# Performance work log

Measured on AMD Instinct MI355X. Metric: run time of the kernel, lower is better.

The kernel has to match this reference:

```python
import jax, jax.numpy as jnp
import numpy as np

D_MODEL = 1024
H = 16
D_K = D_MODEL // H


def setup_inputs() -> dict:
    key = jax.random.key(0)
    ks = jax.random.split(key, 12)
    b, nq, nk = 2, 2048, 2048
    inp = {
        "queries": jax.random.normal(ks[0], (b, nq, D_MODEL), jnp.float32),
        "keys": jax.random.normal(ks[1], (b, nk, D_MODEL), jnp.float32),
        "values": jax.random.normal(ks[2], (b, nk, D_MODEL), jnp.float32),
        "query_mask": jax.random.uniform(ks[3], (b, nq), jnp.float32),
        "key_mask": jax.random.uniform(ks[4], (b, nk), jnp.float32),
        "attention_mask": jax.random.randint(ks[5], (b, 1, nq, nk), 0, 2).astype(bool),
        "attention_weights": jax.random.uniform(ks[6], (b, 1, nq, nk), jnp.float32),
        # Linear params init: normal(std=0.001) weights, zero bias (per init_weights)
        "Wq": 0.001 * jax.random.normal(ks[7], (D_MODEL, D_MODEL), jnp.float32),
        "Wk": 0.001 * jax.random.normal(ks[8], (D_MODEL, D_MODEL), jnp.float32),
        "Wv": 0.001 * jax.random.normal(ks[9], (D_MODEL, D_MODEL), jnp.float32),
        "Wo": 0.001 * jax.random.normal(ks[10], (D_MODEL, D_MODEL), jnp.float32),
        "bq": jnp.zeros((D_MODEL,), jnp.float32),
        "bk": jnp.zeros((D_MODEL,), jnp.float32),
        "bv": jnp.zeros((D_MODEL,), jnp.float32),
        "bo": jnp.zeros((D_MODEL,), jnp.float32),
    }
    return inp


def reference(queries, keys, values, query_mask, key_mask, attention_mask,
              attention_weights, Wq, Wk, Wv, Wo, bq, bk, bv, bo):
    b, nq, _ = queries.shape
    nk = keys.shape[1]
    # projections (torch Linear: x @ W.T + b)
    q = (queries @ Wq.T + bq).reshape(b, nq, H, D_K).transpose(0, 2, 1, 3)  # bhqd
    k = (keys @ Wk.T + bk).reshape(b, nk, H, D_K).transpose(0, 2, 1, 3)    # bhkd
    v = (values @ Wv.T + bv).reshape(b, nk, H, D_K).transpose(0, 2, 1, 3)  # bhkd
    # multiplicative per-token masks
    q = q * query_mask[:, None, :, None]
    k = k * key_mask[:, None, :, None]
    v = v * key_mask[:, None, :, None]
    att = jnp.einsum('bhqd,bhkd->bhqk', q, k) / np.sqrt(D_K).astype(np.float32)
    att = att * attention_weights
    att = jnp.where(attention_mask, -jnp.inf, att)
    att_softmax = jax.nn.softmax(att, axis=-1)
    # dropout is identity in eval/reference mode
    out = jnp.einsum('bhqk,bhkd->bhqd', att_softmax, v)
    out = out.transpose(0, 2, 1, 3).reshape(b, nq, H * D_K)
    out_final = out @ Wo.T + bo
    return (out_final, att_softmax)
```

## Files before the change

kernel.cpp:

```cpp
#include <hip/hip_runtime.h>

#define B2 2
#define NQ 2048
#define NK 2048
#define DM 1024
#define NH 16
#define DK 64
#define KC 64

typedef unsigned short u16;
typedef __attribute__((ext_vector_type(8))) short bf16x8;
typedef __attribute__((ext_vector_type(4))) float f32x4;

__device__ __forceinline__ u16 f2bf(float f) {
  unsigned u = __float_as_uint(f);
  u += 0x7FFFu + ((u >> 16) & 1u);
  return (u16)(u >> 16);
}
__device__ __forceinline__ float bf2f(u16 u) {
  return __uint_as_float(((unsigned)u) << 16);
}

#if __has_builtin(__builtin_amdgcn_exp2f)
#define EXP2F(x) __builtin_amdgcn_exp2f(x)
#else
#define EXP2F(x) exp2f(x)
#endif

#define MFMA(a, b, c) __builtin_amdgcn_mfma_f32_16x16x32_bf16(a, b, c, 0, 0, 0)

#define EXPC 0.18033688011112043f

__global__ __launch_bounds__(256) void k_convert(
    const float* __restrict__ s0, const float* __restrict__ s1, const float* __restrict__ s2,
    const float* __restrict__ s3, const float* __restrict__ s4, const float* __restrict__ s5,
    const float* __restrict__ s6,
    u16* __restrict__ d0, u16* __restrict__ d1, u16* __restrict__ d2, u16* __restrict__ d3,
    u16* __restrict__ d4, u16* __restrict__ d5, u16* __restrict__ d6,
    const float* __restrict__ attw, const int* __restrict__ amask, u16* __restrict__ fw) {
  const int j = blockIdx.y;
  if (j == 7) {
    const int i = (blockIdx.x * 256 + threadIdx.x) * 8;
#pragma unroll
    for (int hh = 0; hh < 2; hh++) {
      const float4 w = *(const float4*)(attw + i + 4 * hh);
      const int4 m = *(const int4*)(amask + i + 4 * hh);
      ushort4 o;
      o.x = m.x ? 0x7FC0 : f2bf(w.x);
      o.y = m.y ? 0x7FC0 : f2bf(w.y);
      o.z = m.z ? 0x7FC0 : f2bf(w.z);
      o.w = m.w ? 0x7FC0 : f2bf(w.w);
      *(ushort4*)(fw + i + 4 * hh) = o;
    }
    return;
  }
  const int n = (j < 3) ? (4 * 1024 * 1024) : (1024 * 1024);
  const int i = (blockIdx.x * 256 + threadIdx.x) * 4;
  if (i >= n) return;
  const float* s = (j == 0) ? s0 : (j == 1) ? s1 : (j == 2) ? s2 : (j == 3) ? s3
                  : (j == 4) ? s4 : (j == 5) ? s5 : s6;
  u16* d = (j == 0) ? d0 : (j == 1) ? d1 : (j == 2) ? d2 : (j == 3) ? d3
          : (j == 4) ? d4 : (j == 5) ? d5 : d6;
  const float4 f = *(const float4*)(s + i);
  ushort4 o;
  o.x = f2bf(f.x); o.y = f2bf(f.y); o.z = f2bf(f.z); o.w = f2bf(f.w);
  *(ushort4*)(d + i) = o;
}

__device__ __forceinline__ void gemm_core(
    const u16* __restrict__ A, const u16* __restrict__ Wm,
    int tm, int tn, u16* As, u16* Bs, f32x4 acc[4][4]) {
  const int tid = threadIdx.x;
  const int lane = tid & 63;
  const int wid = tid >> 6;
  const int wm = (wid >> 1) * 64, wn = (wid & 1) * 64;
  const int cc = lane & 15, gg = lane >> 4;
  const int srow = tid >> 2, scol = 8 * (tid & 3);
  const size_t ra0 = (size_t)(tm + srow) * DM + scol;
  const size_t ra1 = (size_t)(tm + 64 + srow) * DM + scol;
  const size_t rb0 = (size_t)(tn + srow) * DM + scol;
  const size_t rb1 = (size_t)(tn + 64 + srow) * DM + scol;
  const f32x4 Z4 = {0.f, 0.f, 0.f, 0.f};
#pragma unroll
  for (int i = 0; i < 4; i++)
#pragma unroll
    for (int j = 0; j < 4; j++) acc[i][j] = Z4;

  *(bf16x8*)&As[tid * 8]        = *(const bf16x8*)(A + ra0);
  *(bf16x8*)&As[2048 + tid * 8] = *(const bf16x8*)(A + ra1);
  *(bf16x8*)&Bs[tid * 8]        = *(const bf16x8*)(Wm + rb0);
  *(bf16x8*)&Bs[2048 + tid * 8] = *(const bf16x8*)(Wm + rb1);

  int buf = 0;
  for (int kk = 0; kk < DM; kk += 32) {
    __syncthreads();
    const int o = buf * 4096;
    bf16x8 af[4], bv[4];
#pragma unroll
    for (int i = 0; i < 4; i++) af[i] = *(const bf16x8*)&As[o + (wm + i * 16 + cc) * 32 + 8 * gg];
#pragma unroll
    for (int i = 0; i < 4; i++) bv[i] = *(const bf16x8*)&Bs[o + (wn + i * 16 + cc) * 32 + 8 * gg];
    if (kk + 32 < DM) {
      const int p = (buf ^ 1) * 4096;
      *(bf16x8*)&As[p + tid * 8]        = *(const bf16x8*)(A + ra0 + kk + 32);
      *(bf16x8*)&As[p + 2048 + tid * 8] = *(const bf16x8*)(A + ra1 + kk + 32);
      *(bf16x8*)&Bs[p + tid * 8]        = *(const bf16x8*)(Wm + rb0 + kk + 32);
      *(bf16x8*)&Bs[p + 2048 + tid * 8] = *(const bf16x8*)(Wm + rb1 + kk + 32);
    }
#pragma unroll
    for (int mi = 0; mi < 4; mi++)
#pragma unroll
      for (int ni = 0; ni < 4; ni++) acc[mi][ni] = MFMA(af[mi], bv[ni], acc[mi][ni]);
    buf ^= 1;
  }
}

__global__ __launch_bounds__(256) void k_proj(
    const u16* __restrict__ xq, const u16* __restrict__ xk, const u16* __restrict__ xv,
    const u16* __restrict__ wqb, const u16* __restrict__ wkb, const u16* __restrict__ wvb,
    const float* __restrict__ bq, const float* __restrict__ bk, const float* __restrict__ bv,
    const float* __restrict__ qmask, const float* __restrict__ kmask,
    u16* __restrict__ q_ws, u16* __restrict__ k_ws, u16* __restrict__ vT_ws) {
  __shared__ u16 As[2 * 4096];
  __shared__ u16 Bs[2 * 4096];
  const int z = blockIdx.z;
  const u16* A = (z == 0) ? xq : (z == 1) ? xk : xv;
  const u16* Wm = (z == 0) ? wqb : (z == 1) ? wkb : wvb;
  const float* bias = (z == 0) ? bq : (z == 1) ? bk : bv;
  const float* rmask = (z == 0) ? qmask : kmask;
  const int tm = blockIdx.x * 128, tn = blockIdx.y * 128;
  f32x4 acc[4][4];
  gemm_core(A, Wm, tm, tn, As, Bs, acc);

  const int lane = threadIdx.x & 63;
  const int wid = threadIdx.x >> 6;
  const int wm = (wid >> 1) * 64, wn = (wid & 1) * 64;
  const int cc = lane & 15, gg = lane >> 4;
  const int b = tm >> 11;
  const int tok0 = tm & 2047;
#pragma unroll
  for (int mi = 0; mi < 4; mi++) {
    const int rl = wm + mi * 16 + 4 * gg;
    float rm[4];
#pragma unroll
    for (int r = 0; r < 4; r++) rm[r] = rmask[b * NQ + tok0 + rl + r];
#pragma unroll
    for (int ni = 0; ni < 4; ni++) {
      const int col = tn + wn + ni * 16 + cc;
      const int h = col >> 6, d = col & 63;
      const float bs = bias[col];
      f32x4 a = acc[mi][ni];
      if (z <= 1) {
        u16* dst = ((z == 0) ? q_ws : k_ws) +
                   ((size_t)(b * NH + h) * NQ + tok0 + rl) * DK + d;
#pragma unroll
        for (int r = 0; r < 4; r++) dst[(size_t)r * DK] = f2bf((a[r] + bs) * rm[r]);
      } else {
        ushort4 pk;
        pk.x = f2bf((a[0] + bs) * rm[0]);
        pk.y = f2bf((a[1] + bs) * rm[1]);
        pk.z = f2bf((a[2] + bs) * rm[2]);
        pk.w = f2bf((a[3] + bs) * rm[3]);
        *(ushort4*)(vT_ws + ((size_t)(b * NH + h) * DK + d) * NK + tok0 + rl) = pk;
      }
    }
  }
}

__global__ __launch_bounds__(256) void k_attn(
    const u16* __restrict__ q_ws, const u16* __restrict__ k_ws, const u16* __restrict__ vT_ws,
    const u16* __restrict__ fw, float* __restrict__ att_out, u16* __restrict__ ctxb) {
  __shared__ u16 Ks[128][72];
  __shared__ u16 Ps[4][16][72];
  const int bh = blockIdx.y;
  const int b = bh >> 4, hh = bh & 15;
  const int qb = blockIdx.x * 64;
  const int tid = threadIdx.x, lane = tid & 63, wid = tid >> 6;
  const int cc = lane & 15, gg = lane >> 4;
  const int qr0 = qb + wid * 16;
  const u16* qp = q_ws + ((size_t)bh * NQ + qr0 + cc) * DK + 8 * gg;
  const bf16x8 aq0 = *(const bf16x8*)qp;
  const bf16x8 aq1 = *(const bf16x8*)(qp + 32);
  const u16* fwrow = fw + ((size_t)b * NQ + qr0 + cc) * NK;
  const f32x4 Z4 = {0.f, 0.f, 0.f, 0.f};
  const int sr = tid >> 3, sc = 8 * (tid & 7);

  float sum = 0.f;
  for (int kc = 0; kc < NK; kc += 128) {
#pragma unroll
    for (int i = 0; i < 4; i++)
      *(bf16x8*)&Ks[i * 32 + sr][sc] =
          *(const bf16x8*)(k_ws + ((size_t)bh * NK + kc + i * 32 + sr) * DK + sc);
    __syncthreads();
#pragma unroll
    for (int n = 0; n < 8; n++) {
      const bf16x8 k0 = *(const bf16x8*)&Ks[n * 16 + cc][8 * gg];
      const bf16x8 k1 = *(const bf16x8*)&Ks[n * 16 + cc][32 + 8 * gg];
      f32x4 acc = Z4;
      acc = MFMA(k0, aq0, acc);
      acc = MFMA(k1, aq1, acc);
      const int k0i = kc + n * 16 + 4 * gg;
      const ushort4 fv = *(const ushort4*)(fwrow + k0i);
      const float e0 = EXP2F(acc[0] * bf2f(fv.x) * EXPC);
      const float e1 = EXP2F(acc[1] * bf2f(fv.y) * EXPC);
      const float e2 = EXP2F(acc[2] * bf2f(fv.z) * EXPC);
      const float e3 = EXP2F(acc[3] * bf2f(fv.w) * EXPC);
      sum += (e0 == e0) ? e0 : 0.f;
      sum += (e1 == e1) ? e1 : 0.f;
      sum += (e2 == e2) ? e2 : 0.f;
      sum += (e3 == e3) ? e3 : 0.f;
    }
    __syncthreads();
  }
  sum += __shfl_xor(sum, 16);
  sum += __shfl_xor(sum, 32);
  const float rinv = (sum > 0.f) ? 1.0f / sum : 0.f;

  f32x4 o[4];
#pragma unroll
  for (int i = 0; i < 4; i++) o[i] = Z4;
  float* attrow = att_out + (size_t)bh * NQ * NK + (size_t)(qr0 + cc) * NK;

  for (int kc = 0; kc < NK; kc += KC) {
#pragma unroll
    for (int i = 0; i < 2; i++) {
      *(bf16x8*)&Ks[i * 32 + sr][sc] =
          *(const bf16x8*)(k_ws + ((size_t)bh * NK + kc + i * 32 + sr) * DK + sc);
      *(bf16x8*)&Ks[64 + i * 32 + sr][sc] =
          *(const bf16x8*)(vT_ws + ((size_t)bh * DK + i * 32 + sr) * NK + kc + sc);
    }
    __syncthreads();
#pragma unroll
    for (int n = 0; n < 4; n++) {
      const bf16x8 k0 = *(const bf16x8*)&Ks[n * 16 + cc][8 * gg];
      const bf16x8 k1 = *(const bf16x8*)&Ks[n * 16 + cc][32 + 8 * gg];
      f32x4 acc = Z4;
      acc = MFMA(k0, aq0, acc);
      acc = MFMA(k1, aq1, acc);
      const int k0i = kc + n * 16 + 4 * gg;
      const ushort4 fv = *(const ushort4*)(fwrow + k0i);
      const float e0 = EXP2F(acc[0] * bf2f(fv.x) * EXPC);
      const float e1 = EXP2F(acc[1] * bf2f(fv.y) * EXPC);
      const float e2 = EXP2F(acc[2] * bf2f(fv.z) * EXPC);
      const float e3 = EXP2F(acc[3] * bf2f(fv.w) * EXPC);
      f32x4 pv;
      pv.x = (e0 == e0) ? e0 * rinv : 0.f;
      pv.y = (e1 == e1) ? e1 * rinv : 0.f;
      pv.z = (e2 == e2) ? e2 * rinv : 0.f;
      pv.w = (e3 == e3) ? e3 * rinv : 0.f;
      __builtin_nontemporal_store(pv, (f32x4*)(attrow + k0i));
      ushort4 pk;
      pk.x = f2bf(pv.x); pk.y = f2bf(pv.y); pk.z = f2bf(pv.z); pk.w = f2bf(pv.w);
      *(ushort4*)&Ps[wid][cc][n * 16 + 4 * gg] = pk;
    }
    const bf16x8 pa0 = *(const bf16x8*)&Ps[wid][cc][8 * gg];
    const bf16x8 pa1 = *(const bf16x8*)&Ps[wid][cc][32 + 8 * gg];
#pragma unroll
    for (int nd = 0; nd < 4; nd++) {
      const bf16x8 vb0 = *(const bf16x8*)&Ks[64 + nd * 16 + cc][8 * gg];
      const bf16x8 vb1 = *(const bf16x8*)&Ks[64 + nd * 16 + cc][32 + 8 * gg];
      o[nd] = MFMA(pa0, vb0, o[nd]);
      o[nd] = MFMA(pa1, vb1, o[nd]);
    }
    __syncthreads();
  }
#pragma unroll
  for (int nd = 0; nd < 4; nd++)
#pragma unroll
    for (int r = 0; r < 4; r++)
      ctxb[((size_t)b * NQ + qr0 + 4 * gg + r) * DM + hh * 64 + nd * 16 + cc] = f2bf(o[nd][r]);
}

__global__ __launch_bounds__(256) void k_oproj(
    const u16* __restrict__ ctxb, const u16* __restrict__ wob,
    const float* __restrict__ bo, float* __restrict__ outp) {
  __shared__ u16 As[2 * 4096];
  __shared__ u16 Bs[2 * 4096];
  const int tm = blockIdx.x * 128, tn = blockIdx.y * 128;
  f32x4 acc[4][4];
  gemm_core(ctxb, wob, tm, tn, As, Bs, acc);
  const int lane = threadIdx.x & 63;
  const int wid = threadIdx.x >> 6;
  const int wm = (wid >> 1) * 64, wn = (wid & 1) * 64;
  const int cc = lane & 15, gg = lane >> 4;
#pragma unroll
  for (int mi = 0; mi < 4; mi++) {
    const int rl = tm + wm + mi * 16 + 4 * gg;
#pragma unroll
    for (int ni = 0; ni < 4; ni++) {
      const int col = tn + wn + ni * 16 + cc;
      const float bs = bo[col];
      f32x4 a = acc[mi][ni];
#pragma unroll
      for (int r = 0; r < 4; r++) outp[(size_t)(rl + r) * DM + col] = a[r] + bs;
    }
  }
}

extern "C" void kernel_launch(void* const* d_in, const int* in_sizes, int n_in,
                              void* d_out, int out_size, void* d_ws, size_t ws_size,
                              hipStream_t stream) {
  (void)in_sizes; (void)n_in; (void)out_size; (void)ws_size;
  const float* queries = (const float*)d_in[0];
  const float* keys    = (const float*)d_in[1];
  const float* values  = (const float*)d_in[2];
  const float* qmask   = (const float*)d_in[3];
  const float* kmask   = (const float*)d_in[4];
  const int*   amask   = (const int*)d_in[5];
  const float* attw    = (const float*)d_in[6];
  const float* Wq = (const float*)d_in[7];
  const float* Wk = (const float*)d_in[8];
  const float* Wv = (const float*)d_in[9];
  const float* Wo = (const float*)d_in[10];
  const float* bq = (const float*)d_in[11];
  const float* bk = (const float*)d_in[12];
  const float* bv = (const float*)d_in[13];
  const float* bo = (const float*)d_in[14];

  float* outf = (float*)d_out;
  float* att_out = outf + (size_t)4194304;

  char* p = (char*)d_ws;
  u16* q_ws  = (u16*)p; p += (size_t)4194304 * 2;
  u16* k_ws  = (u16*)p; p += (size_t)4194304 * 2;
  u16* vT_ws = (u16*)p; p += (size_t)4194304 * 2;
  u16* ctxb  = (u16*)p; p += (size_t)4194304 * 2;
  u16* wob   = (u16*)p; p += (size_t)1048576 * 2;
  u16* fw    = (u16*)p; p += (size_t)8388608 * 2;

  char* t = (char*)att_out;
  u16* xq  = (u16*)t; t += (size_t)4194304 * 2;
  u16* xk  = (u16*)t; t += (size_t)4194304 * 2;
  u16* xv  = (u16*)t; t += (size_t)4194304 * 2;
  u16* wqb = (u16*)t; t += (size_t)1048576 * 2;
  u16* wkb = (u16*)t; t += (size_t)1048576 * 2;
  u16* wvb = (u16*)t; t += (size_t)1048576 * 2;

  k_convert<<<dim3(4096, 8, 1), 256, 0, stream>>>(queries, keys, values, Wq, Wk, Wv, Wo,
                                                  xq, xk, xv, wqb, wkb, wvb, wob,
                                                  attw, amask, fw);
  k_proj<<<dim3(32, 8, 3), 256, 0, stream>>>(xq, xk, xv, wqb, wkb, wvb, bq, bk, bv,
                                             qmask, kmask, q_ws, k_ws, vT_ws);
  k_attn<<<dim3(32, 32, 1), 256, 0, stream>>>(q_ws, k_ws, vT_ws, fw, att_out, ctxb);
  k_oproj<<<dim3(32, 8, 1), 256, 0, stream>>>(ctxb, wob, bo, outf);
}
```

Baseline: 326.9 us.

## Fuse fp32-to-bf16 conversion into GEMM loads, swizzle grids, widen attention blocks

Removes the separate conversion pass for inputs and weights. The projection and output GEMMs now read fp32 directly and convert to bf16 while staging tiles into shared memory. All kernels get XCD-aware block-index swizzling. The attention kernel doubles to 512 threads with 128 queries per block, so each K/V tile is reused by more queries, and MFMA sections get s_setprio hints. The trade-off is twice the global bytes per GEMM tile load, plus the conversion work repeated across every tile that reads the same data.

```diff
diff --git a/kernel.cpp b/kernel.cpp
--- a/kernel.cpp
+++ b/kernel.cpp
@@ -20,6 +20,16 @@
 __device__ __forceinline__ float bf2f(u16 u) {
   return __uint_as_float(((unsigned)u) << 16);
 }
+__device__ __forceinline__ bf16x8 ld8f(const float* __restrict__ p) {
+  const float4 a = *(const float4*)p;
+  const float4 b = *(const float4*)(p + 4);
+  bf16x8 v;
+  v[0] = (short)f2bf(a.x); v[1] = (short)f2bf(a.y);
+  v[2] = (short)f2bf(a.z); v[3] = (short)f2bf(a.w);
+  v[4] = (short)f2bf(b.x); v[5] = (short)f2bf(b.y);
+  v[6] = (short)f2bf(b.z); v[7] = (short)f2bf(b.w);
+  return v;
+}
 
 #if __has_builtin(__builtin_amdgcn_exp2f)
 #define EXP2F(x) __builtin_amdgcn_exp2f(x)
@@ -31,44 +41,25 @@
 
 #define EXPC 0.18033688011112043f
 
-__global__ __launch_bounds__(256) void k_convert(
-    const float* __restrict__ s0, const float* __restrict__ s1, const float* __restrict__ s2,
-    const float* __restrict__ s3, const float* __restrict__ s4, const float* __restrict__ s5,
-    const float* __restrict__ s6,
-    u16* __restrict__ d0, u16* __restrict__ d1, u16* __restrict__ d2, u16* __restrict__ d3,
-    u16* __restrict__ d4, u16* __restrict__ d5, u16* __restrict__ d6,
+__global__ __launch_bounds__(256) void k_fw(
     const float* __restrict__ attw, const int* __restrict__ amask, u16* __restrict__ fw) {
-  const int j = blockIdx.y;
-  if (j == 7) {
-    const int i = (blockIdx.x * 256 + threadIdx.x) * 8;
-#pragma unroll
-    for (int hh = 0; hh < 2; hh++) {
-      const float4 w = *(const float4*)(attw + i + 4 * hh);
-      const int4 m = *(const int4*)(amask + i + 4 * hh);
-      ushort4 o;
-      o.x = m.x ? 0x7FC0 : f2bf(w.x);
-      o.y = m.y ? 0x7FC0 : f2bf(w.y);
-      o.z = m.z ? 0x7FC0 : f2bf(w.z);
-      o.w = m.w ? 0x7FC0 : f2bf(w.w);
-      *(ushort4*)(fw + i + 4 * hh) = o;
-    }
-    return;
-  }
-  const int n = (j < 3) ? (4 * 1024 * 1024) : (1024 * 1024);
-  const int i = (blockIdx.x * 256 + threadIdx.x) * 4;
-  if (i >= n) return;
-  const float* s = (j == 0) ? s0 : (j == 1) ? s1 : (j == 2) ? s2 : (j == 3) ? s3
-                  : (j == 4) ? s4 : (j == 5) ? s5 : s6;
-  u16* d = (j == 0) ? d0 : (j == 1) ? d1 : (j == 2) ? d2 : (j == 3) ? d3
-          : (j == 4) ? d4 : (j == 5) ? d5 : d6;
-  const float4 f = *(const float4*)(s + i);
-  ushort4 o;
-  o.x = f2bf(f.x); o.y = f2bf(f.y); o.z = f2bf(f.z); o.w = f2bf(f.w);
-  *(ushort4*)(d + i) = o;
-}
-
+  const int i = (blockIdx.x * 256 + threadIdx.x) * 8;
+#pragma unroll
+  for (int hh = 0; hh < 2; hh++) {
+    const float4 w = *(const float4*)(attw + i + 4 * hh);
+    const int4 m = *(const int4*)(amask + i + 4 * hh);
+    ushort4 o;
+    o.x = m.x ? 0x7FC0 : f2bf(w.x);
+    o.y = m.y ? 0x7FC0 : f2bf(w.y);
+    o.z = m.z ? 0x7FC0 : f2bf(w.z);
+    o.w = m.w ? 0x7FC0 : f2bf(w.w);
+    *(ushort4*)(fw + i + 4 * hh) = o;
+  }
+}
+
+template <bool AF32, bool WF32>
 __device__ __forceinline__ void gemm_core(
-    const u16* __restrict__ A, const u16* __restrict__ Wm,
+    const void* __restrict__ Ap, const void* __restrict__ Wp,
     int tm, int tn, u16* As, u16* Bs, f32x4 acc[4][4]) {
   const int tid = threadIdx.x;
   const int lane = tid & 63;
@@ -80,16 +71,20 @@
   const size_t ra1 = (size_t)(tm + 64 + srow) * DM + scol;
   const size_t rb0 = (size_t)(tn + srow) * DM + scol;
   const size_t rb1 = (size_t)(tn + 64 + srow) * DM + scol;
+  const float* Af = (const float*)Ap; const u16* Ab = (const u16*)Ap;
+  const float* Wf = (const float*)Wp; const u16* Wb = (const u16*)Wp;
   const f32x4 Z4 = {0.f, 0.f, 0.f, 0.f};
 #pragma unroll
   for (int i = 0; i < 4; i++)
 #pragma unroll
     for (int j = 0; j < 4; j++) acc[i][j] = Z4;
 
-  *(bf16x8*)&As[tid * 8]        = *(const bf16x8*)(A + ra0);
-  *(bf16x8*)&As[2048 + tid * 8] = *(const bf16x8*)(A + ra1);
-  *(bf16x8*)&Bs[tid * 8]        = *(const bf16x8*)(Wm + rb0);
-  *(bf16x8*)&Bs[2048 + tid * 8] = *(const bf16x8*)(Wm + rb1);
+#define LD_A(off) (AF32 ? ld8f(Af + (off)) : *(const bf16x8*)(Ab + (off)))
+#define LD_W(off) (WF32 ? ld8f(Wf + (off)) : *(const bf16x8*)(Wb + (off)))
+  *(bf16x8*)&As[tid * 8]        = LD_A(ra0);
+  *(bf16x8*)&As[2048 + tid * 8] = LD_A(ra1);
+  *(bf16x8*)&Bs[tid * 8]        = LD_W(rb0);
+  *(bf16x8*)&Bs[2048 + tid * 8] = LD_W(rb1);
 
   int buf = 0;
   for (int kk = 0; kk < DM; kk += 32) {
@@ -102,10 +97,10 @@
     for (int i = 0; i < 4; i++) bv[i] = *(const bf16x8*)&Bs[o + (wn + i * 16 + cc) * 32 + 8 * gg];
     if (kk + 32 < DM) {
       const int p = (buf ^ 1) * 4096;
-      *(bf16x8*)&As[p + tid * 8]        = *(const bf16x8*)(A + ra0 + kk + 32);
-      *(bf16x8*)&As[p + 2048 + tid * 8] = *(const bf16x8*)(A + ra1 + kk + 32);
-      *(bf16x8*)&Bs[p + tid * 8]        = *(const bf16x8*)(Wm + rb0 + kk + 32);
-      *(bf16x8*)&Bs[p + 2048 + tid * 8] = *(const bf16x8*)(Wm + rb1 + kk + 32);
+      *(bf16x8*)&As[p + tid * 8]        = LD_A(ra0 + kk + 32);
+      *(bf16x8*)&As[p + 2048 + tid * 8] = LD_A(ra1 + kk + 32);
+      *(bf16x8*)&Bs[p + tid * 8]        = LD_W(rb0 + kk + 32);
+      *(bf16x8*)&Bs[p + 2048 + tid * 8] = LD_W(rb1 + kk + 32);
     }
 #pragma unroll
     for (int mi = 0; mi < 4; mi++)
@@ -113,24 +108,30 @@
       for (int ni = 0; ni < 4; ni++) acc[mi][ni] = MFMA(af[mi], bv[ni], acc[mi][ni]);
     buf ^= 1;
   }
+#undef LD_A
+#undef LD_W
 }
 
 __global__ __launch_bounds__(256) void k_proj(
-    const u16* __restrict__ xq, const u16* __restrict__ xk, const u16* __restrict__ xv,
-    const u16* __restrict__ wqb, const u16* __restrict__ wkb, const u16* __restrict__ wvb,
+    const float* __restrict__ xq, const float* __restrict__ xk, const float* __restrict__ xv,
+    const float* __restrict__ wq, const float* __restrict__ wk, const float* __restrict__ wv,
     const float* __restrict__ bq, const float* __restrict__ bk, const float* __restrict__ bv,
     const float* __restrict__ qmask, const float* __restrict__ kmask,
     u16* __restrict__ q_ws, u16* __restrict__ k_ws, u16* __restrict__ vT_ws) {
   __shared__ u16 As[2 * 4096];
   __shared__ u16 Bs[2 * 4096];
-  const int z = blockIdx.z;
-  const u16* A = (z == 0) ? xq : (z == 1) ? xk : xv;
-  const u16* Wm = (z == 0) ? wqb : (z == 1) ? wkb : wvb;
+  const int bid = blockIdx.x;
+  const int swz = (bid & 7) * 96 + (bid >> 3);
+  const int tm = (swz & 31) * 128;
+  const int yz = swz >> 5;
+  const int tn = (yz & 7) * 128;
+  const int z = yz >> 3;
+  const float* A = (z == 0) ? xq : (z == 1) ? xk : xv;
+  const float* Wm = (z == 0) ? wq : (z == 1) ? wk : wv;
   const float* bias = (z == 0) ? bq : (z == 1) ? bk : bv;
   const float* rmask = (z == 0) ? qmask : kmask;
-  const int tm = blockIdx.x * 128, tn = blockIdx.y * 128;
   f32x4 acc[4][4];
-  gemm_core(A, Wm, tm, tn, As, Bs, acc);
+  gemm_core<true, true>(A, Wm, tm, tn, As, Bs, acc);
 
   const int lane = threadIdx.x & 63;
   const int wid = threadIdx.x >> 6;
@@ -167,14 +168,16 @@
   }
 }
 
-__global__ __launch_bounds__(256) void k_attn(
+__global__ __launch_bounds__(512) void k_attn(
     const u16* __restrict__ q_ws, const u16* __restrict__ k_ws, const u16* __restrict__ vT_ws,
     const u16* __restrict__ fw, float* __restrict__ att_out, u16* __restrict__ ctxb) {
   __shared__ u16 Ks[128][72];
-  __shared__ u16 Ps[4][16][72];
-  const int bh = blockIdx.y;
+  __shared__ u16 Ps[8][16][72];
+  const int bid = blockIdx.x;
+  const int swz = ((bid & 7) << 6) + (bid >> 3);
+  const int bh = swz >> 4;
+  const int qb = (swz & 15) << 7;
   const int b = bh >> 4, hh = bh & 15;
-  const int qb = blockIdx.x * 64;
   const int tid = threadIdx.x, lane = tid & 63, wid = tid >> 6;
   const int cc = lane & 15, gg = lane >> 4;
   const int qr0 = qb + wid * 16;
@@ -187,18 +190,20 @@
 
   float sum = 0.f;
   for (int kc = 0; kc < NK; kc += 128) {
-#pragma unroll
-    for (int i = 0; i < 4; i++)
-      *(bf16x8*)&Ks[i * 32 + sr][sc] =
-          *(const bf16x8*)(k_ws + ((size_t)bh * NK + kc + i * 32 + sr) * DK + sc);
+    *(bf16x8*)&Ks[sr][sc] =
+        *(const bf16x8*)(k_ws + ((size_t)bh * NK + kc + sr) * DK + sc);
+    *(bf16x8*)&Ks[64 + sr][sc] =
+        *(const bf16x8*)(k_ws + ((size_t)bh * NK + kc + 64 + sr) * DK + sc);
     __syncthreads();
 #pragma unroll
     for (int n = 0; n < 8; n++) {
       const bf16x8 k0 = *(const bf16x8*)&Ks[n * 16 + cc][8 * gg];
       const bf16x8 k1 = *(const bf16x8*)&Ks[n * 16 + cc][32 + 8 * gg];
       f32x4 acc = Z4;
+      __builtin_amdgcn_s_setprio(1);
       acc = MFMA(k0, aq0, acc);
       acc = MFMA(k1, aq1, acc);
+      __builtin_amdgcn_s_setprio(0);
       const int k0i = kc + n * 16 + 4 * gg;
       const ushort4 fv = *(const ushort4*)(fwrow + k0i);
       const float e0 = EXP2F(acc[0] * bf2f(fv.x) * EXPC);
@@ -222,21 +227,20 @@
   float* attrow = att_out + (size_t)bh * NQ * NK + (size_t)(qr0 + cc) * NK;
 
   for (int kc = 0; kc < NK; kc += KC) {
-#pragma unroll
-    for (int i = 0; i < 2; i++) {
-      *(bf16x8*)&Ks[i * 32 + sr][sc] =
-          *(const bf16x8*)(k_ws + ((size_t)bh * NK + kc + i * 32 + sr) * DK + sc);
-      *(bf16x8*)&Ks[64 + i * 32 + sr][sc] =
-          *(const bf16x8*)(vT_ws + ((size_t)bh * DK + i * 32 + sr) * NK + kc + sc);
-    }
+    *(bf16x8*)&Ks[sr][sc] =
+        *(const bf16x8*)(k_ws + ((size_t)bh * NK + kc + sr) * DK + sc);
+    *(bf16x8*)&Ks[64 + sr][sc] =
+        *(const bf16x8*)(vT_ws + ((size_t)bh * DK + sr) * NK + kc + sc);
     __syncthreads();
 #pragma unroll
     for (int n = 0; n < 4; n++) {
       const bf16x8 k0 = *(const bf16x8*)&Ks[n * 16 + cc][8 * gg];
       const bf16x8 k1 = *(const bf16x8*)&Ks[n * 16 + cc][32 + 8 * gg];
       f32x4 acc = Z4;
+      __builtin_amdgcn_s_setprio(1);
       acc = MFMA(k0, aq0, acc);
       acc = MFMA(k1, aq1, acc);
+      __builtin_amdgcn_s_setprio(0);
       const int k0i = kc + n * 16 + 4 * gg;
       const ushort4 fv = *(const ushort4*)(fwrow + k0i);
       const float e0 = EXP2F(acc[0] * bf2f(fv.x) * EXPC);
@@ -255,6 +259,7 @@
     }
     const bf16x8 pa0 = *(const bf16x8*)&Ps[wid][cc][8 * gg];
     const bf16x8 pa1 = *(const bf16x8*)&Ps[wid][cc][32 + 8 * gg];
+    __builtin_amdgcn_s_setprio(1);
 #pragma unroll
     for (int nd = 0; nd < 4; nd++) {
       const bf16x8 vb0 = *(const bf16x8*)&Ks[64 + nd * 16 + cc][8 * gg];
@@ -262,6 +267,7 @@
       o[nd] = MFMA(pa0, vb0, o[nd]);
       o[nd] = MFMA(pa1, vb1, o[nd]);
     }
+    __builtin_amdgcn_s_setprio(0);
     __syncthreads();
   }
 #pragma unroll
@@ -272,13 +278,16 @@
 }
 
 __global__ __launch_bounds__(256) void k_oproj(
-    const u16* __restrict__ ctxb, const u16* __restrict__ wob,
+    const u16* __restrict__ ctxb, const float* __restrict__ wo,
     const float* __restrict__ bo, float* __restrict__ outp) {
   __shared__ u16 As[2 * 4096];
   __shared__ u16 Bs[2 * 4096];
-  const int tm = blockIdx.x * 128, tn = blockIdx.y * 128;
+  const int bid = blockIdx.x;
+  const int swz = ((bid & 7) << 5) + (bid >> 3);
+  const int tm = (swz & 31) * 128;
+  const int tn = (swz >> 5) * 128;
   f32x4 acc[4][4];
-  gemm_core(ctxb, wob, tm, tn, As, Bs, acc);
+  gemm_core<false, true>(ctxb, wo, tm, tn, As, Bs, acc);
   const int lane = threadIdx.x & 63;
   const int wid = threadIdx.x >> 6;
   const int wm = (wid >> 1) * 64, wn = (wid & 1) * 64;
@@ -325,22 +334,12 @@
   u16* k_ws  = (u16*)p; p += (size_t)4194304 * 2;
   u16* vT_ws = (u16*)p; p += (size_t)4194304 * 2;
   u16* ctxb  = (u16*)p; p += (size_t)4194304 * 2;
-  u16* wob   = (u16*)p; p += (size_t)1048576 * 2;
   u16* fw    = (u16*)p; p += (size_t)8388608 * 2;
 
-  char* t = (char*)att_out;
-  u16* xq  = (u16*)t; t += (size_t)4194304 * 2;
-  u16* xk  = (u16*)t; t += (size_t)4194304 * 2;
-  u16* xv  = (u16*)t; t += (size_t)4194304 * 2;
-  u16* wqb = (u16*)t; t += (size_t)1048576 * 2;
-  u16* wkb = (u16*)t; t += (size_t)1048576 * 2;
-  u16* wvb = (u16*)t; t += (size_t)1048576 * 2;
-
-  k_convert<<<dim3(4096, 8, 1), 256, 0, stream>>>(queries, keys, values, Wq, Wk, Wv, Wo,
-                                                  xq, xk, xv, wqb, wkb, wvb, wob,
-                                                  attw, amask, fw);
-  k_proj<<<dim3(32, 8, 3), 256, 0, stream>>>(xq, xk, xv, wqb, wkb, wvb, bq, bk, bv,
-                                             qmask, kmask, q_ws, k_ws, vT_ws);
-  k_attn<<<dim3(32, 32, 1), 256, 0, stream>>>(q_ws, k_ws, vT_ws, fw, att_out, ctxb);
-  k_oproj<<<dim3(32, 8, 1), 256, 0, stream>>>(ctxb, wob, bo, outf);
-}
+  k_fw<<<dim3(4096, 1, 1), 256, 0, stream>>>(attw, amask, fw);
+  k_proj<<<dim3(768, 1, 1), 256, 0, stream>>>(queries, keys, values, Wq, Wk, Wv,
+                                              bq, bk, bv, qmask, kmask,
+                                              q_ws, k_ws, vT_ws);
+  k_attn<<<dim3(512, 1, 1), 512, 0, stream>>>(q_ws, k_ws, vT_ws, fw, att_out, ctxb);
+  k_oproj<<<dim3(256, 1, 1), 256, 0, stream>>>(ctxb, Wo, bo, outf);
+}
```

Result: slower. 429.9 us (+31.5%).
